# Kernel optimization log

Hardware: AMD Instinct MI355X
Metric: run time of the kernel (lower is better)

The kernel has to match this reference:

```python
import jax, jax.numpy as jnp
import numpy as np

N_HIDDEN = 32
RANK = 6
SV_DECAY_GAMMA = 0.3
LEAK_ALPHA = 0.1
INPUT_DIM = 64
OUTPUT_DIM = 32


def setup_inputs() -> dict:
    key = jax.random.key(0)
    ks = jax.random.split(key, 8)
    B, T = 256, 2048
    inputs = jax.random.normal(ks[0], (B, T, INPUT_DIM), dtype=jnp.float32)
    # parameters (match torch init scales)
    m = jax.random.normal(ks[1], (N_HIDDEN, 1), dtype=jnp.float32) * 0.1
    n = jax.random.normal(ks[2], (N_HIDDEN, 1), dtype=jnp.float32) * 0.1
    M = jax.random.normal(ks[3], (N_HIDDEN, RANK), dtype=jnp.float32) * 0.1
    Nmat = jax.random.normal(ks[4], (N_HIDDEN, RANK), dtype=jnp.float32) * 0.1
    # singular-value-decay scaling of M, N (as in _initialize_with_sv_decay)
    target_sv = jnp.exp(-SV_DECAY_GAMMA * jnp.arange(RANK, dtype=jnp.float32))
    target_sv = target_sv / target_sv.sum() * RANK
    sqrt_sv = jnp.sqrt(target_sv)
    M = M * sqrt_sv[None, :]
    Nmat = Nmat * sqrt_sv[None, :]
    bias = jnp.zeros((N_HIDDEN,), dtype=jnp.float32)
    # W_in: Linear(input_dim, N, bias=False) -> weight [N, input_dim]
    lim_in = 1.0 / np.sqrt(INPUT_DIM)
    W_in = jax.random.uniform(ks[5], (N_HIDDEN, INPUT_DIM), minval=-lim_in, maxval=lim_in, dtype=jnp.float32)
    lim_out = 1.0 / np.sqrt(N_HIDDEN)
    W_out = jax.random.uniform(ks[6], (OUTPUT_DIM, N_HIDDEN), minval=-lim_out, maxval=lim_out, dtype=jnp.float32)
    b_out = jax.random.uniform(ks[7], (OUTPUT_DIM,), minval=-lim_out, maxval=lim_out, dtype=jnp.float32)
    return {"inputs": inputs, "W_in": W_in, "m": m, "n": n, "M": M,
            "Nmat": Nmat, "bias": bias, "W_out": W_out, "b_out": b_out}


def reference(inputs, W_in, m, n, M, Nmat, bias, W_out, b_out):
    # h_{t+1} = (1-a) h_t + a * tanh(W_rec h_t + W_in u_t + b); y_t = W_out h_t + b_out
    B, T, _ = inputs.shape
    alpha = LEAK_ALPHA
    # W_rec = m n^T + M N^T (time-invariant; torch recomputes per step, same math)
    W_rec = m @ n.T + M @ Nmat.T                         # [N, N]
    x_proj = jnp.einsum('bti,ni->btn', inputs, W_in)     # [B, T, N]
    h0 = jnp.zeros((B, N_HIDDEN), dtype=inputs.dtype)

    def step(h, x_t):
        pre = h @ W_rec.T + x_t + bias
        h_new = (1.0 - alpha) * h + alpha * jnp.tanh(pre)
        return h_new, h_new

    h_final, hs = jax.lax.scan(step, h0, jnp.swapaxes(x_proj, 0, 1))  # hs: [T, B, N]
    outputs = jnp.einsum('tbn,on->bto', hs, W_out) + b_out            # [B, T, O]
    return outputs, h_final
```

## Files before the change

### kernel.cpp

```cpp
#include <hip/hip_runtime.h>

#define RNN_B 256
#define RNN_T 2048
#define RNN_IN 64
#define RNN_N 32
#define RNN_O 32
#define RNN_R 6
#define RNN_ALPHA 0.1f
#define KSCALE 2.8853900817779268f

__global__ __launch_bounds__(256) void k_xproj(
    const float* __restrict__ u, const float* __restrict__ W_in,
    const float* __restrict__ bias, float* __restrict__ xp)
{
    const int tid = blockIdx.x * 256 + threadIdx.x;
    const float4* __restrict__ u4 =
        reinterpret_cast<const float4*>(u) + (size_t)tid * (RNN_IN / 4);
    float acc[RNN_N];
    #pragma unroll
    for (int n = 0; n < RNN_N; ++n) acc[n] = bias[n];
    #pragma unroll
    for (int q = 0; q < RNN_IN / 4; ++q) {
        const float4 v = u4[q];
        #pragma unroll
        for (int n = 0; n < RNN_N; ++n) {
            const float* wr = W_in + n * RNN_IN + 4 * q;
            acc[n] = fmaf(wr[0], v.x, acc[n]);
            acc[n] = fmaf(wr[1], v.y, acc[n]);
            acc[n] = fmaf(wr[2], v.z, acc[n]);
            acc[n] = fmaf(wr[3], v.w, acc[n]);
        }
    }
    float4* __restrict__ o4 =
        reinterpret_cast<float4*>(xp) + (size_t)tid * (RNN_N / 4);
    #pragma unroll
    for (int q = 0; q < RNN_N / 4; ++q)
        o4[q] = make_float4(KSCALE * acc[4*q+0], KSCALE * acc[4*q+1],
                            KSCALE * acc[4*q+2], KSCALE * acc[4*q+3]);
}

template <int CTRL>
__device__ __forceinline__ float dpp_add(float v) {
    int t = __builtin_amdgcn_update_dpp(0, __float_as_int(v), CTRL, 0xf, 0xf, true);
    return v + __int_as_float(t);
}
__device__ __forceinline__ float sum16(float v) {
    v = dpp_add<0xB1>(v);
    v = dpp_add<0x4E>(v);
    v = dpp_add<0x141>(v);
    v = dpp_add<0x140>(v);
    return v;
}

__device__ __forceinline__ float fast_exp2(float x) {
#if __has_builtin(__builtin_amdgcn_exp2f)
    return __builtin_amdgcn_exp2f(x);
#else
    return __expf(x * 0.6931471805599453f);
#endif
}
__device__ __forceinline__ float fast_rcp(float x) {
#if __has_builtin(__builtin_amdgcn_rcpf)
    return __builtin_amdgcn_rcpf(x);
#else
    return __frcp_rn(x);
#endif
}

__global__ __launch_bounds__(64, 1) void k_recur(
    const float* __restrict__ m, const float* __restrict__ nvec,
    const float* __restrict__ Mmat, const float* __restrict__ Nmat,
    const float* __restrict__ xp,
    float* __restrict__ hout,
    float* __restrict__ hfin)
{
    const int b    = blockIdx.x;
    const int lane = threadIdx.x;
    const int k    = lane & 15;
    const int iA   = 2 * k;
    const int iB   = 2 * k + 1;

    float cNA[RNN_R + 1], cNB[RNN_R + 1];
    cNA[0] = nvec[iA];  cNB[0] = nvec[iB];
    #pragma unroll
    for (int r = 0; r < RNN_R; ++r) {
        cNA[r+1] = Nmat[iA*RNN_R + r];
        cNB[r+1] = Nmat[iB*RNN_R + r];
    }
    float cMA[RNN_R + 1], cMB[RNN_R + 1];
    cMA[0] = KSCALE * m[iA];  cMB[0] = KSCALE * m[iB];
    #pragma unroll
    for (int r = 0; r < RNN_R; ++r) {
        cMA[r+1] = KSCALE * Mmat[iA*RNN_R + r];
        cMB[r+1] = KSCALE * Mmat[iB*RNN_R + r];
    }

    const float2* __restrict__ x2 =
        reinterpret_cast<const float2*>(xp + (size_t)b * (RNN_T * RNN_N)) + k;
    float2* __restrict__ h2 =
        reinterpret_cast<float2*>(hout + (size_t)b * (RNN_T * RNN_N));

    float hA = 0.0f, hB = 0.0f;

    const int PF = 8;
    float2 xr[PF];
    #pragma unroll
    for (int i = 0; i < PF; ++i) xr[i] = x2[i * (RNN_N / 2)];

    #pragma unroll 8
    for (int t = 0; t < RNN_T; ++t) {
        const float xA = xr[0].x, xB = xr[0].y;
        #pragma unroll
        for (int i = 0; i < PF - 1; ++i) xr[i] = xr[i + 1];
        xr[PF - 1] = x2[(t + PF) * (RNN_N / 2)];

        float s[RNN_R + 1];
        #pragma unroll
        for (int r = 0; r < RNN_R + 1; ++r)
            s[r] = sum16(fmaf(hB, cNB[r], hA * cNA[r]));

        float zA0 = fmaf(cMA[0], s[0], xA);
        float zB0 = fmaf(cMB[0], s[0], xB);
        float zA1 = cMA[1] * s[1];
        float zB1 = cMB[1] * s[1];
        zA0 = fmaf(cMA[2], s[2], zA0);  zB0 = fmaf(cMB[2], s[2], zB0);
        zA1 = fmaf(cMA[3], s[3], zA1);  zB1 = fmaf(cMB[3], s[3], zB1);
        zA0 = fmaf(cMA[4], s[4], zA0);  zB0 = fmaf(cMB[4], s[4], zB0);
        zA1 = fmaf(cMA[5], s[5], zA1);  zB1 = fmaf(cMB[5], s[5], zB1);
        zA0 = fmaf(cMA[6], s[6], zA0);  zB0 = fmaf(cMB[6], s[6], zB0);
        const float zA = zA0 + zA1, zB = zB0 + zB1;

        const float eA = fast_exp2(zA), eB = fast_exp2(zB);
        const float gA = fmaf(1.0f - RNN_ALPHA, hA, RNN_ALPHA);
        const float gB = fmaf(1.0f - RNN_ALPHA, hB, RNN_ALPHA);
        hA = fmaf(-2.0f * RNN_ALPHA, fast_rcp(eA + 1.0f), gA);
        hB = fmaf(-2.0f * RNN_ALPHA, fast_rcp(eB + 1.0f), gB);

        if (lane < 16) h2[t * (RNN_N / 2) + lane] = make_float2(hA, hB);
    }
    if (lane < 16)
        reinterpret_cast<float2*>(hfin + (size_t)b * RNN_N)[lane] =
            make_float2(hA, hB);
}

__global__ __launch_bounds__(256) void k_out(
    const float* __restrict__ W_out, const float* __restrict__ b_out,
    const float* __restrict__ hsrc, float* __restrict__ ydst)
{
    const int tid = blockIdx.x * 256 + threadIdx.x;
    const float4* __restrict__ p4 =
        reinterpret_cast<const float4*>(hsrc) + (size_t)tid * (RNN_N / 4);
    float4* __restrict__ q4 =
        reinterpret_cast<float4*>(ydst) + (size_t)tid * (RNN_N / 4);
    float y[RNN_O];
    #pragma unroll
    for (int o = 0; o < RNN_O; ++o) y[o] = b_out[o];
    #pragma unroll
    for (int q = 0; q < RNN_N / 4; ++q) {
        const float4 v = p4[q];
        #pragma unroll
        for (int o = 0; o < RNN_O; ++o) {
            const float* wr = W_out + o * RNN_N + 4 * q;
            y[o] = fmaf(wr[0], v.x, y[o]);
            y[o] = fmaf(wr[1], v.y, y[o]);
            y[o] = fmaf(wr[2], v.z, y[o]);
            y[o] = fmaf(wr[3], v.w, y[o]);
        }
    }
    #pragma unroll
    for (int q = 0; q < RNN_N / 4; ++q)
        q4[q] = make_float4(y[4*q+0], y[4*q+1], y[4*q+2], y[4*q+3]);
}

extern "C" void kernel_launch(void* const* d_in, const int* in_sizes, int n_in,
                              void* d_out, int out_size, void* d_ws, size_t ws_size,
                              hipStream_t stream)
{
    const float* u     = (const float*)d_in[0];
    const float* W_in  = (const float*)d_in[1];
    const float* m     = (const float*)d_in[2];
    const float* nvec  = (const float*)d_in[3];
    const float* Mmat  = (const float*)d_in[4];
    const float* Nmat  = (const float*)d_in[5];
    const float* bias  = (const float*)d_in[6];
    const float* W_out = (const float*)d_in[7];
    const float* b_out = (const float*)d_in[8];
    float* out = (float*)d_out;

    float* hfin = out + (size_t)RNN_B * RNN_T * RNN_N;

    const size_t hbytes = (size_t)RNN_B * RNN_T * RNN_N * sizeof(float);
    float* hbuf = (ws_size >= hbytes) ? (float*)d_ws : out;

    k_xproj<<<(RNN_B * RNN_T) / 256, 256, 0, stream>>>(u, W_in, bias, out);
    k_recur<<<RNN_B, 64, 0, stream>>>(m, nvec, Mmat, Nmat, out, hbuf, hfin);
    k_out  <<<(RNN_B * RNN_T) / 256, 256, 0, stream>>>(W_out, b_out, hbuf, out);
}
```

Baseline: 713.4 us.

## Split rank reductions across wave halves and combine with permlane32 swap

The 7 rank-1 projections (padded to 8) are now divided between the two 32-lane halves of the wavefront, four per half, instead of every lane computing all seven. Each half runs its four DPP reductions interleaved, and the partial pre-activations are merged across halves with permlane32_swap, falling back to a shuffle. This shortens the serial per-step dependency chain of the recurrence, at the cost of one extra cross-half exchange per step plus a masking multiply on the input term.

```diff
diff --git a/kernel.cpp b/kernel.cpp
--- a/kernel.cpp
+++ b/kernel.cpp
@@ -44,12 +44,16 @@
     int t = __builtin_amdgcn_update_dpp(0, __float_as_int(v), CTRL, 0xf, 0xf, true);
     return v + __int_as_float(t);
 }
-__device__ __forceinline__ float sum16(float v) {
-    v = dpp_add<0xB1>(v);
-    v = dpp_add<0x4E>(v);
-    v = dpp_add<0x141>(v);
-    v = dpp_add<0x140>(v);
-    return v;
+
+__device__ __forceinline__ float xhalf_sum(float v) {
+#if __has_builtin(__builtin_amdgcn_permlane32_swap)
+    typedef int v2i __attribute__((ext_vector_type(2)));
+    v2i r = __builtin_amdgcn_permlane32_swap(__float_as_int(v),
+                                             __float_as_int(v), false, false);
+    return __int_as_float(r.x) + __int_as_float(r.y);
+#else
+    return v + __shfl_xor(v, 32, 64);
+#endif
 }
 
 __device__ __forceinline__ float fast_exp2(float x) {
@@ -79,21 +83,23 @@
     const int k    = lane & 15;
     const int iA   = 2 * k;
     const int iB   = 2 * k + 1;
-
-    float cNA[RNN_R + 1], cNB[RNN_R + 1];
-    cNA[0] = nvec[iA];  cNB[0] = nvec[iB];
-    #pragma unroll
-    for (int r = 0; r < RNN_R; ++r) {
-        cNA[r+1] = Nmat[iA*RNN_R + r];
-        cNB[r+1] = Nmat[iB*RNN_R + r];
-    }
-    float cMA[RNN_R + 1], cMB[RNN_R + 1];
-    cMA[0] = KSCALE * m[iA];  cMB[0] = KSCALE * m[iB];
-    #pragma unroll
-    for (int r = 0; r < RNN_R; ++r) {
-        cMA[r+1] = KSCALE * Mmat[iA*RNN_R + r];
-        cMB[r+1] = KSCALE * Mmat[iB*RNN_R + r];
-    }
+    const int half = (lane >> 5) & 1;
+
+    float cnA[4], cnB[4], cmA[4], cmB[4];
+    #pragma unroll
+    for (int j = 0; j < 4; ++j) {
+        const int r = 4 * half + j;
+        if (r == 0) {
+            cnA[j] = nvec[iA];              cnB[j] = nvec[iB];
+            cmA[j] = KSCALE * m[iA];        cmB[j] = KSCALE * m[iB];
+        } else if (r <= RNN_R) {
+            cnA[j] = Nmat[iA*RNN_R + (r-1)];          cnB[j] = Nmat[iB*RNN_R + (r-1)];
+            cmA[j] = KSCALE * Mmat[iA*RNN_R + (r-1)]; cmB[j] = KSCALE * Mmat[iB*RNN_R + (r-1)];
+        } else {
+            cnA[j] = 0.f; cnB[j] = 0.f; cmA[j] = 0.f; cmB[j] = 0.f;
+        }
+    }
+    const float xmask = (half == 0) ? 1.0f : 0.0f;
 
     const float2* __restrict__ x2 =
         reinterpret_cast<const float2*>(xp + (size_t)b * (RNN_T * RNN_N)) + k;
@@ -114,21 +120,25 @@
         for (int i = 0; i < PF - 1; ++i) xr[i] = xr[i + 1];
         xr[PF - 1] = x2[(t + PF) * (RNN_N / 2)];
 
-        float s[RNN_R + 1];
-        #pragma unroll
-        for (int r = 0; r < RNN_R + 1; ++r)
-            s[r] = sum16(fmaf(hB, cNB[r], hA * cNA[r]));
-
-        float zA0 = fmaf(cMA[0], s[0], xA);
-        float zB0 = fmaf(cMB[0], s[0], xB);
-        float zA1 = cMA[1] * s[1];
-        float zB1 = cMB[1] * s[1];
-        zA0 = fmaf(cMA[2], s[2], zA0);  zB0 = fmaf(cMB[2], s[2], zB0);
-        zA1 = fmaf(cMA[3], s[3], zA1);  zB1 = fmaf(cMB[3], s[3], zB1);
-        zA0 = fmaf(cMA[4], s[4], zA0);  zB0 = fmaf(cMB[4], s[4], zB0);
-        zA1 = fmaf(cMA[5], s[5], zA1);  zB1 = fmaf(cMB[5], s[5], zB1);
-        zA0 = fmaf(cMA[6], s[6], zA0);  zB0 = fmaf(cMB[6], s[6], zB0);
-        const float zA = zA0 + zA1, zB = zB0 + zB1;
+        float s0 = fmaf(hB, cnB[0], hA * cnA[0]);
+        float s1 = fmaf(hB, cnB[1], hA * cnA[1]);
+        float s2 = fmaf(hB, cnB[2], hA * cnA[2]);
+        float s3 = fmaf(hB, cnB[3], hA * cnA[3]);
+        s0 = dpp_add<0xB1>(s0);  s1 = dpp_add<0xB1>(s1);
+        s2 = dpp_add<0xB1>(s2);  s3 = dpp_add<0xB1>(s3);
+        s0 = dpp_add<0x4E>(s0);  s1 = dpp_add<0x4E>(s1);
+        s2 = dpp_add<0x4E>(s2);  s3 = dpp_add<0x4E>(s3);
+        s0 = dpp_add<0x141>(s0); s1 = dpp_add<0x141>(s1);
+        s2 = dpp_add<0x141>(s2); s3 = dpp_add<0x141>(s3);
+        s0 = dpp_add<0x140>(s0); s1 = dpp_add<0x140>(s1);
+        s2 = dpp_add<0x140>(s2); s3 = dpp_add<0x140>(s3);
+
+        float tA = fmaf(cmA[0], s0, fmaf(cmA[1], s1, xA * xmask));
+        float tB = fmaf(cmB[0], s0, fmaf(cmB[1], s1, xB * xmask));
+        float uA = fmaf(cmA[2], s2, cmA[3] * s3);
+        float uB = fmaf(cmB[2], s2, cmB[3] * s3);
+        const float zA = xhalf_sum(tA + uA);
+        const float zB = xhalf_sum(tB + uB);
 
         const float eA = fast_exp2(zA), eB = fast_exp2(zB);
         const float gA = fmaf(1.0f - RNN_ALPHA, hA, RNN_ALPHA);
```

Measured after the change: 608.4 us. 14.7% less time.
